# Performance work log

Measured on AMD Instinct MI355X. Metric: run time of the kernel, lower is better.

The kernel has to match this reference:

```python
import jax, jax.numpy as jnp
import numpy as np

EPS = 1e-12  # matches torch F.normalize eps

def _l2_normalize(x):
    n = jnp.linalg.norm(x, axis=-1, keepdims=True)
    return x / jnp.maximum(n, EPS)

def setup_inputs() -> dict:
    key = jax.random.key(0)
    k1, k2, k3 = jax.random.split(key, 3)
    B, D, C = 2048, 1024, 65536
    return {
        "query": jax.random.normal(k1, (B, D), dtype=jnp.float32),
        "memory_keys": jax.random.normal(k2, (C, D), dtype=jnp.float32),
        "memory_values": jax.random.normal(k3, (C, D), dtype=jnp.float32),
        "memory_usage": jnp.zeros((C,), dtype=jnp.float32),
        "k": 8,
    }

def reference(query, memory_keys, memory_values, memory_usage, k):
    # cosine similarity: [B, C]
    qn = _l2_normalize(query)
    mn = _l2_normalize(memory_keys)
    sims = jnp.matmul(qn, mn.T)
    # top-k indices per query: [B, k]
    _, indices = jax.lax.top_k(sims, k)
    # gather retrieved keys/values: [B, k, D]
    retrieved_keys = memory_keys[indices]
    retrieved_values = memory_values[indices]
    # usage scatter-add (+1 per retrieved slot), vectorized form of the loop
    capacity = memory_usage.shape[0]
    counts = jax.ops.segment_sum(
        jnp.ones(indices.size, dtype=memory_usage.dtype),
        indices.reshape(-1),
        num_segments=capacity,
    )
    usage_new = memory_usage + counts
    return retrieved_keys, retrieved_values, usage_new
```

## Files before the change

kernel.cpp:

```cpp
#include <hip/hip_runtime.h>
#include <math.h>

#define BQ 2048
#define DD 1024
#define CC 65536
#define KSEL 8
#define NSTRIPE 32
#define SC (CC / NSTRIPE)
#define GTM 128
#define GTN 128
#define GBK 32
#define NTILES (SC / GTN)
#define LCAND 8
#define TRES 32

typedef unsigned int u32;
typedef unsigned short ushort_t;
typedef __attribute__((ext_vector_type(8))) short bf16x8;
typedef __attribute__((ext_vector_type(4))) float f32x4;


__device__ __forceinline__ ushort_t f2bf(float f) {
    u32 u = __builtin_bit_cast(u32, f);
    return (ushort_t)((u + 0x7FFFu + ((u >> 16) & 1u)) >> 16);
}

__device__ __forceinline__ void gl_lds16(const ushort_t* g, ushort_t* l) {
    __builtin_amdgcn_global_load_lds(
        (const __attribute__((address_space(1))) u32*)g,
        (__attribute__((address_space(3))) u32*)l, 16, 0, 0);
}

__global__ __launch_bounds__(256) void norms_kernel(
    const float* __restrict__ q, const float* __restrict__ keys,
    double* __restrict__ qinv, double* __restrict__ kinv)
{
    const int gtid = blockIdx.x * 256 + threadIdx.x;
    const int wave = gtid >> 6;
    const int lane = threadIdx.x & 63;
    const float4* src;
    double* dst;
    if (wave < CC) {
        src = (const float4*)(keys + (size_t)wave * DD);
        dst = kinv + wave;
    } else {
        const int r = wave - CC;
        if (r >= BQ) return;
        src = (const float4*)(q + (size_t)r * DD);
        dst = qinv + r;
    }
    double s = 0.0;
#pragma unroll
    for (int u = 0; u < 4; ++u) {
        float4 v = src[lane + 64 * u];
        s += (double)v.x * v.x + (double)v.y * v.y +
             (double)v.z * v.z + (double)v.w * v.w;
    }
    for (int off = 32; off > 0; off >>= 1) s += __shfl_down(s, off);
    if (lane == 0) {
        double n = sqrt(s);
        *dst = 1.0 / fmax(n, 1e-12);
    }
}

__global__ __launch_bounds__(256) void convert_kernel(
    const float* __restrict__ q, const float* __restrict__ keys,
    const double* __restrict__ qinv, const double* __restrict__ kinv,
    ushort_t* __restrict__ qn, ushort_t* __restrict__ kn)
{
    const int row = blockIdx.x;
    const int t = threadIdx.x;
    const float4* src;
    ushort_t* dst;
    float inv;
    if (row < CC) {
        src = (const float4*)(keys + (size_t)row * DD);
        dst = kn + (size_t)row * DD;
        inv = (float)kinv[row];
    } else {
        const int r = row - CC;
        src = (const float4*)(q + (size_t)r * DD);
        dst = qn + (size_t)r * DD;
        inv = (float)qinv[r];
    }
    float4 v = src[t];
    ushort4 o;
    o.x = f2bf(v.x * inv); o.y = f2bf(v.y * inv);
    o.z = f2bf(v.z * inv); o.w = f2bf(v.w * inv);
    ((ushort4*)dst)[t] = o;
}

__global__ __launch_bounds__(256, 2) void gemm_topk_kernel(
    const ushort_t* __restrict__ qn, const ushort_t* __restrict__ kn,
    unsigned* __restrict__ cand)
{
    __shared__ ushort_t As[GTM * GBK];
    __shared__ ushort_t Bs[GTN * GBK];
    __shared__ float tilebuf[GTM][65];

    const int tid = threadIdx.x;
    const int wid = tid >> 6;
    const int lane = tid & 63;
    const int wy = wid >> 1, wx = wid & 1;
    const int l15 = lane & 15, quad = lane >> 4;
    const int m0 = blockIdx.x * GTM;
    const int sbase = blockIdx.y * SC;

    const int e0 = tid, e1 = tid + 256;
    const ushort_t* gA0 = qn + (size_t)(m0 + (e0 >> 2)) * DD + (e0 & 3) * 8;
    const ushort_t* gA1 = qn + (size_t)(m0 + (e1 >> 2)) * DD + (e1 & 3) * 8;
    ushort_t* lA0 = As + e0 * 8;
    ushort_t* lA1 = As + e1 * 8;
    ushort_t* lB0 = Bs + e0 * 8;
    ushort_t* lB1 = Bs + e1 * 8;

    float tv[LCAND];
    int ti[LCAND];
#pragma unroll
    for (int l = 0; l < LCAND; ++l) { tv[l] = -3.0e38f; ti[l] = 0; }
    float minv = -3.0e38f;
    int minpos = 0;

    for (int nt = 0; nt < NTILES; ++nt) {
        const int cbase = sbase + nt * GTN;
        const ushort_t* gB0 = kn + (size_t)(cbase + (e0 >> 2)) * DD + (e0 & 3) * 8;
        const ushort_t* gB1 = kn + (size_t)(cbase + (e1 >> 2)) * DD + (e1 & 3) * 8;

        f32x4 acc[4][4];
#pragma unroll
        for (int i = 0; i < 4; ++i)
#pragma unroll
            for (int j = 0; j < 4; ++j) acc[i][j] = (f32x4)0.0f;

        for (int kt = 0; kt < DD / GBK; ++kt) {
            const int k0 = kt * GBK;
            __syncthreads();
            gl_lds16(gA0 + k0, lA0);
            gl_lds16(gA1 + k0, lA1);
            gl_lds16(gB0 + k0, lB0);
            gl_lds16(gB1 + k0, lB1);
            __syncthreads();

            bf16x8 af[4], bfr[4];
#pragma unroll
            for (int ri = 0; ri < 4; ++ri)
                af[ri] = *(const bf16x8*)(As + (wy * 64 + ri * 16 + l15) * GBK + quad * 8);
#pragma unroll
            for (int ci = 0; ci < 4; ++ci)
                bfr[ci] = *(const bf16x8*)(Bs + (wx * 64 + ci * 16 + l15) * GBK + quad * 8);
#pragma unroll
            for (int ri = 0; ri < 4; ++ri)
#pragma unroll
                for (int ci = 0; ci < 4; ++ci)
                    acc[ri][ci] = __builtin_amdgcn_mfma_f32_16x16x32_bf16(
                        af[ri], bfr[ci], acc[ri][ci], 0, 0, 0);
        }

        for (int cc2 = 0; cc2 < 2; ++cc2) {
            __syncthreads();
            if (wx == cc2) {
#pragma unroll
                for (int ri = 0; ri < 4; ++ri)
#pragma unroll
                    for (int ci = 0; ci < 4; ++ci)
#pragma unroll
                        for (int r = 0; r < 4; ++r)
                            tilebuf[wy * 64 + ri * 16 + quad * 4 + r][ci * 16 + l15] =
                                acc[ri][ci][r];
            }
            __syncthreads();
            if (tid < GTM) {
                const int gc0 = cbase + cc2 * 64;
                for (int j = 0; j < 64; ++j) {
                    float v = tilebuf[tid][j];
                    if (v > minv) {
                        tv[minpos] = v; ti[minpos] = gc0 + j;
                        minv = tv[0]; minpos = 0;
#pragma unroll
                        for (int l = 1; l < LCAND; ++l)
                            if (tv[l] < minv) { minv = tv[l]; minpos = l; }
                    }
                }
            }
        }
    }

    if (tid < GTM) {
        unsigned* dst = cand + (size_t)(m0 + tid) * (NSTRIPE * LCAND) + blockIdx.y * LCAND;
#pragma unroll
        for (int l = 0; l < LCAND; ++l)
            dst[l] = ((unsigned)f2bf(tv[l]) << 16) | (unsigned)(ti[l] & 0xFFFF);
    }
}

__global__ __launch_bounds__(256) void merge_kernel(
    const int* __restrict__ cand, int* __restrict__ sel_idx,
    float* __restrict__ counts)
{
    const int gid = blockIdx.x * 256 + threadIdx.x;
    if (gid < CC) counts[gid] = 0.0f;
    const int row = gid >> 6;
    const int lane = threadIdx.x & 63;
    const int* cv = cand + (size_t)row * (NSTRIPE * LCAND);
    int v[4];
#pragma unroll
    for (int u = 0; u < 4; ++u) v[u] = cv[lane + 64 * u];
    for (int r = 0; r < TRES; ++r) {
        int bv = v[0];
#pragma unroll
        for (int u = 1; u < 4; ++u) bv = max(bv, v[u]);
#pragma unroll
        for (int off = 1; off < 64; off <<= 1) bv = max(bv, __shfl_xor(bv, off));
#pragma unroll
        for (int u = 0; u < 4; ++u)
            if (v[u] == bv) v[u] = (int)0x80000000;
        if (lane == 0) sel_idx[row * TRES + r] = bv & 0xFFFF;
    }
}

__global__ __launch_bounds__(256) void rescore_kernel(
    const float* __restrict__ q, const float* __restrict__ keys,
    const double* __restrict__ qinv, const double* __restrict__ kinv,
    const int* __restrict__ sel_idx, double* __restrict__ sel_val)
{
    const int pair = (blockIdx.x * 256 + threadIdx.x) >> 6;
    const int lane = threadIdx.x & 63;
    const int b = pair >> 5;
    const int c = sel_idx[pair];
    const float4* qr = (const float4*)(q + (size_t)b * DD);
    const float4* kr = (const float4*)(keys + (size_t)c * DD);
    double s = 0.0;
#pragma unroll
    for (int u = 0; u < 4; ++u) {
        float4 a = qr[lane + 64 * u];
        float4 k4 = kr[lane + 64 * u];
        s += (double)a.x * k4.x + (double)a.y * k4.y +
             (double)a.z * k4.z + (double)a.w * k4.w;
    }
    for (int off = 32; off > 0; off >>= 1) s += __shfl_down(s, off);
    if (lane == 0) sel_val[pair] = s * qinv[b] * kinv[c];
}

__global__ __launch_bounds__(256) void finalize_kernel(
    const double* __restrict__ sel_val, const int* __restrict__ sel_idx,
    int* __restrict__ topk_idx, float* __restrict__ counts)
{
    const int b = blockIdx.x * 256 + threadIdx.x;
    if (b >= BQ) return;
    double bv[KSEL]; int bi[KSEL];
#pragma unroll
    for (int j = 0; j < KSEL; ++j) { bv[j] = -1.0e300; bi[j] = 0x7fffffff; }
    for (int t = 0; t < TRES; ++t) {
        double v = sel_val[b * TRES + t];
        int idx = sel_idx[b * TRES + t];
        int p = KSEL;
        while (p > 0 && (v > bv[p - 1] || (v == bv[p - 1] && idx < bi[p - 1]))) --p;
        if (p < KSEL) {
            for (int s = KSEL - 1; s > p; --s) { bv[s] = bv[s - 1]; bi[s] = bi[s - 1]; }
            bv[p] = v; bi[p] = idx;
        }
    }
    for (int j = 0; j < KSEL; ++j) {
        topk_idx[b * KSEL + j] = bi[j];
        atomicAdd(&counts[bi[j]], 1.0f);
    }
}

__global__ __launch_bounds__(256) void gather_kernel(
    const float* __restrict__ keys, const float* __restrict__ values,
    const int* __restrict__ topk_idx, float* __restrict__ out_k,
    float* __restrict__ out_v)
{
    const int pair = blockIdx.x;
    const int c = topk_idx[pair];
    const int t = threadIdx.x;
    const float4* ks = (const float4*)(keys + (size_t)c * DD);
    const float4* vs = (const float4*)(values + (size_t)c * DD);
    float4* ok = (float4*)out_k + (size_t)pair * (DD / 4);
    float4* ov = (float4*)out_v + (size_t)pair * (DD / 4);
    ok[t] = ks[t];
    ov[t] = vs[t];
}

__global__ __launch_bounds__(256) void usage_kernel(
    const float* __restrict__ usage_in, const float* __restrict__ counts,
    float* __restrict__ out_u)
{
    const int c = blockIdx.x * 256 + threadIdx.x;
    out_u[c] = usage_in[c] + counts[c];
}

extern "C" void kernel_launch(void* const* d_in, const int* in_sizes, int n_in,
                              void* d_out, int out_size, void* d_ws, size_t ws_size,
                              hipStream_t stream)
{
    const float* q      = (const float*)d_in[0];
    const float* keys   = (const float*)d_in[1];
    const float* values = (const float*)d_in[2];
    const float* usage  = (const float*)d_in[3];

    char* ws = (char*)d_ws;
    double* qinv     = (double*)(ws + 0);
    double* kinv     = (double*)(ws + 16384);
    ushort_t* qn     = (ushort_t*)(ws + 540672);
    float* counts    = (float*)(ws + 540672);
    int* sel_idx     = (int*)(ws + 802816);
    double* sel_val  = (double*)(ws + 1064960);
    int* topk        = (int*)(ws + 1589248);
    unsigned* cand   = (unsigned*)(ws + 4734976);

    float* out_k = (float*)d_out;
    float* out_v = out_k + (size_t)BQ * KSEL * DD;
    float* out_u = out_v + (size_t)BQ * KSEL * DD;
    ushort_t* kn = (ushort_t*)d_out;

    norms_kernel<<<(CC + BQ) / 4, 256, 0, stream>>>(q, keys, qinv, kinv);

    convert_kernel<<<CC + BQ, 256, 0, stream>>>(q, keys, qinv, kinv, qn, kn);

    dim3 g2(BQ / GTM, NSTRIPE);
    gemm_topk_kernel<<<g2, 256, 0, stream>>>(qn, kn, cand);

    merge_kernel<<<BQ / 4, 256, 0, stream>>>((const int*)cand, sel_idx, counts);

    rescore_kernel<<<(BQ * TRES) / 4, 256, 0, stream>>>(q, keys, qinv, kinv,
                                                        sel_idx, sel_val);

    finalize_kernel<<<BQ / 256, 256, 0, stream>>>(sel_val, sel_idx, topk, counts);

    gather_kernel<<<BQ * KSEL, 256, 0, stream>>>(keys, values, topk, out_k, out_v);

    usage_kernel<<<CC / 256, 256, 0, stream>>>(usage, counts, out_u);
}
```

Baseline: 1.268 ms.

## Fuse norm+convert, double-buffer GEMM LDS with swizzle, split top-k scan across threads

Merges the norm and bf16 conversion kernels into one pass so keys and queries are read once. The GEMM now double-buffers its LDS tiles with async global-to-LDS prefetch of the next k-slice and next N-tile, using vmcnt waits and raw barriers. It also XOR-swizzles the LDS layout to cut bank conflicts, remaps blocks for L2 locality, and raises wave priority around the MFMAs. The per-tile top-k scan uses all 256 threads (two halves of 32 columns each) with a final merge, at the cost of more LDS and fragile hand-written synchronisation.

```diff
diff --git a/kernel.cpp b/kernel.cpp
--- a/kernel.cpp
+++ b/kernel.cpp
@@ -20,6 +20,9 @@
 typedef __attribute__((ext_vector_type(4))) float f32x4;
 
 
+#define FENCE() asm volatile("" ::: "memory")
+#define LGKM0() asm volatile("s_waitcnt lgkmcnt(0)" ::: "memory")
+
 __device__ __forceinline__ ushort_t f2bf(float f) {
     u32 u = __builtin_bit_cast(u32, f);
     return (ushort_t)((u + 0x7FFFu + ((u >> 16) & 1u)) >> 16);
@@ -31,62 +34,34 @@
         (__attribute__((address_space(3))) u32*)l, 16, 0, 0);
 }
 
-__global__ __launch_bounds__(256) void norms_kernel(
+__global__ __launch_bounds__(256) void normconv_kernel(
     const float* __restrict__ q, const float* __restrict__ keys,
-    double* __restrict__ qinv, double* __restrict__ kinv)
-{
-    const int gtid = blockIdx.x * 256 + threadIdx.x;
-    const int wave = gtid >> 6;
-    const int lane = threadIdx.x & 63;
-    const float4* src;
-    double* dst;
-    if (wave < CC) {
-        src = (const float4*)(keys + (size_t)wave * DD);
-        dst = kinv + wave;
-    } else {
-        const int r = wave - CC;
-        if (r >= BQ) return;
-        src = (const float4*)(q + (size_t)r * DD);
-        dst = qinv + r;
-    }
-    double s = 0.0;
-#pragma unroll
-    for (int u = 0; u < 4; ++u) {
-        float4 v = src[lane + 64 * u];
-        s += (double)v.x * v.x + (double)v.y * v.y +
-             (double)v.z * v.z + (double)v.w * v.w;
-    }
-    for (int off = 32; off > 0; off >>= 1) s += __shfl_down(s, off);
-    if (lane == 0) {
-        double n = sqrt(s);
-        *dst = 1.0 / fmax(n, 1e-12);
-    }
-}
-
-__global__ __launch_bounds__(256) void convert_kernel(
-    const float* __restrict__ q, const float* __restrict__ keys,
-    const double* __restrict__ qinv, const double* __restrict__ kinv,
+    double* __restrict__ qinv, double* __restrict__ kinv,
     ushort_t* __restrict__ qn, ushort_t* __restrict__ kn)
 {
+    __shared__ double red[4];
     const int row = blockIdx.x;
     const int t = threadIdx.x;
-    const float4* src;
-    ushort_t* dst;
-    float inv;
-    if (row < CC) {
-        src = (const float4*)(keys + (size_t)row * DD);
-        dst = kn + (size_t)row * DD;
-        inv = (float)kinv[row];
-    } else {
-        const int r = row - CC;
-        src = (const float4*)(q + (size_t)r * DD);
-        dst = qn + (size_t)r * DD;
-        inv = (float)qinv[r];
-    }
-    float4 v = src[t];
+    const bool iskey = row < CC;
+    const float* src = iskey ? keys + (size_t)row * DD
+                             : q + (size_t)(row - CC) * DD;
+    float4 v = ((const float4*)src)[t];
+    double s = (double)v.x * v.x + (double)v.y * v.y +
+               (double)v.z * v.z + (double)v.w * v.w;
+    for (int off = 32; off > 0; off >>= 1) s += __shfl_down(s, off);
+    if ((t & 63) == 0) red[t >> 6] = s;
+    __syncthreads();
+    const double tot = red[0] + red[1] + red[2] + red[3];
+    const double inv = 1.0 / fmax(sqrt(tot), 1e-12);
+    if (t == 0) {
+        if (iskey) kinv[row] = inv; else qinv[row - CC] = inv;
+    }
+    const float invf = (float)inv;
     ushort4 o;
-    o.x = f2bf(v.x * inv); o.y = f2bf(v.y * inv);
-    o.z = f2bf(v.z * inv); o.w = f2bf(v.w * inv);
+    o.x = f2bf(v.x * invf); o.y = f2bf(v.y * invf);
+    o.z = f2bf(v.z * invf); o.w = f2bf(v.w * invf);
+    ushort_t* dst = iskey ? kn + (size_t)row * DD
+                          : qn + (size_t)(row - CC) * DD;
     ((ushort4*)dst)[t] = o;
 }
 
@@ -94,8 +69,8 @@
     const ushort_t* __restrict__ qn, const ushort_t* __restrict__ kn,
     unsigned* __restrict__ cand)
 {
-    __shared__ ushort_t As[GTM * GBK];
-    __shared__ ushort_t Bs[GTN * GBK];
+    __shared__ ushort_t As[2][GTM * GBK];
+    __shared__ ushort_t Bs[2][GTN * GBK];
     __shared__ float tilebuf[GTM][65];
 
     const int tid = threadIdx.x;
@@ -103,16 +78,27 @@
     const int lane = tid & 63;
     const int wy = wid >> 1, wx = wid & 1;
     const int l15 = lane & 15, quad = lane >> 4;
-    const int m0 = blockIdx.x * GTM;
-    const int sbase = blockIdx.y * SC;
+
+    const int flat = blockIdx.y * 16 + blockIdx.x;
+    const int swz  = (flat & 7) * 64 + (flat >> 3);
+    const int bx = swz & 15, by = swz >> 4;
+    const int m0 = bx * GTM;
+    const int sbase = by * SC;
 
     const int e0 = tid, e1 = tid + 256;
-    const ushort_t* gA0 = qn + (size_t)(m0 + (e0 >> 2)) * DD + (e0 & 3) * 8;
-    const ushort_t* gA1 = qn + (size_t)(m0 + (e1 >> 2)) * DD + (e1 & 3) * 8;
-    ushort_t* lA0 = As + e0 * 8;
-    ushort_t* lA1 = As + e1 * 8;
-    ushort_t* lB0 = Bs + e0 * 8;
-    ushort_t* lB1 = Bs + e1 * 8;
+    const int ks0 = (((e0 & 3) ^ ((e0 >> 3) & 3)) * 8);
+    const int ks1 = (((e1 & 3) ^ ((e1 >> 3) & 3)) * 8);
+    const ushort_t* gA0 = qn + (size_t)(m0 + (e0 >> 2)) * DD + ks0;
+    const ushort_t* gA1 = qn + (size_t)(m0 + (e1 >> 2)) * DD + ks1;
+    const ushort_t* gB0 = kn + (size_t)(sbase + (e0 >> 2)) * DD + ks0;
+    const ushort_t* gB1 = kn + (size_t)(sbase + (e1 >> 2)) * DD + ks1;
+
+#define STAGE(buf, k0_) do {                         \
+        gl_lds16(gA0 + (k0_), As[buf] + e0 * 8);     \
+        gl_lds16(gA1 + (k0_), As[buf] + e1 * 8);     \
+        gl_lds16(gB0 + (k0_), Bs[buf] + e0 * 8);     \
+        gl_lds16(gB1 + (k0_), Bs[buf] + e1 * 8);     \
+    } while (0)
 
     float tv[LCAND];
     int ti[LCAND];
@@ -121,10 +107,12 @@
     float minv = -3.0e38f;
     int minpos = 0;
 
+    const int swz15 = (l15 >> 1) & 3;
+
+    STAGE(0, 0);
+
     for (int nt = 0; nt < NTILES; ++nt) {
         const int cbase = sbase + nt * GTN;
-        const ushort_t* gB0 = kn + (size_t)(cbase + (e0 >> 2)) * DD + (e0 & 3) * 8;
-        const ushort_t* gB1 = kn + (size_t)(cbase + (e1 >> 2)) * DD + (e1 & 3) * 8;
 
         f32x4 acc[4][4];
 #pragma unroll
@@ -132,32 +120,50 @@
 #pragma unroll
             for (int j = 0; j < 4; ++j) acc[i][j] = (f32x4)0.0f;
 
+#pragma unroll 2
         for (int kt = 0; kt < DD / GBK; ++kt) {
-            const int k0 = kt * GBK;
-            __syncthreads();
-            gl_lds16(gA0 + k0, lA0);
-            gl_lds16(gA1 + k0, lA1);
-            gl_lds16(gB0 + k0, lB0);
-            gl_lds16(gB1 + k0, lB1);
-            __syncthreads();
+            const int cur = kt & 1;
+            if (kt < DD / GBK - 1) {
+                STAGE(cur ^ 1, (kt + 1) * GBK);
+                asm volatile("s_waitcnt vmcnt(4)" ::: "memory");
+            } else if (nt < NTILES - 1) {
+                gB0 += (size_t)GTN * DD;
+                gB1 += (size_t)GTN * DD;
+                STAGE(cur ^ 1, 0);
+                asm volatile("s_waitcnt vmcnt(4)" ::: "memory");
+            } else {
+                asm volatile("s_waitcnt vmcnt(0)" ::: "memory");
+            }
+            __builtin_amdgcn_s_barrier();
+            FENCE();
+            __builtin_amdgcn_s_setprio(1);
 
             bf16x8 af[4], bfr[4];
 #pragma unroll
             for (int ri = 0; ri < 4; ++ri)
-                af[ri] = *(const bf16x8*)(As + (wy * 64 + ri * 16 + l15) * GBK + quad * 8);
+                af[ri] = *(const bf16x8*)(As[cur] +
+                    (wy * 64 + ri * 16 + l15) * GBK + ((quad ^ swz15) * 8));
 #pragma unroll
             for (int ci = 0; ci < 4; ++ci)
-                bfr[ci] = *(const bf16x8*)(Bs + (wx * 64 + ci * 16 + l15) * GBK + quad * 8);
+                bfr[ci] = *(const bf16x8*)(Bs[cur] +
+                    (wx * 64 + ci * 16 + l15) * GBK + ((quad ^ swz15) * 8));
 #pragma unroll
             for (int ri = 0; ri < 4; ++ri)
 #pragma unroll
                 for (int ci = 0; ci < 4; ++ci)
                     acc[ri][ci] = __builtin_amdgcn_mfma_f32_16x16x32_bf16(
                         af[ri], bfr[ci], acc[ri][ci], 0, 0, 0);
+
+            __builtin_amdgcn_s_setprio(0);
+            FENCE();
+            __builtin_amdgcn_s_barrier();
+            FENCE();
         }
 
         for (int cc2 = 0; cc2 < 2; ++cc2) {
-            __syncthreads();
+            LGKM0();
+            __builtin_amdgcn_s_barrier();
+            FENCE();
             if (wx == cc2) {
 #pragma unroll
                 for (int ri = 0; ri < 4; ++ri)
@@ -168,11 +174,15 @@
                             tilebuf[wy * 64 + ri * 16 + quad * 4 + r][ci * 16 + l15] =
                                 acc[ri][ci][r];
             }
-            __syncthreads();
-            if (tid < GTM) {
-                const int gc0 = cbase + cc2 * 64;
-                for (int j = 0; j < 64; ++j) {
-                    float v = tilebuf[tid][j];
+            LGKM0();
+            __builtin_amdgcn_s_barrier();
+            FENCE();
+            {
+                const int rr = tid & 127;
+                const int jb = (tid >> 7) << 5;
+                const int gc0 = cbase + cc2 * 64 + jb;
+                for (int j = 0; j < 32; ++j) {
+                    float v = tilebuf[rr][jb + j];
                     if (v > minv) {
                         tv[minpos] = v; ti[minpos] = gc0 + j;
                         minv = tv[0]; minpos = 0;
@@ -185,12 +195,39 @@
         }
     }
 
+    LGKM0();
+    __builtin_amdgcn_s_barrier();
+    FENCE();
+    if (tid >= 128) {
+        const int r2 = tid - 128;
+#pragma unroll
+        for (int l = 0; l < LCAND; ++l) {
+            tilebuf[r2][l] = tv[l];
+            tilebuf[r2][16 + l] = __int_as_float(ti[l]);
+        }
+    }
+    LGKM0();
+    __builtin_amdgcn_s_barrier();
+    FENCE();
     if (tid < GTM) {
-        unsigned* dst = cand + (size_t)(m0 + tid) * (NSTRIPE * LCAND) + blockIdx.y * LCAND;
+#pragma unroll
+        for (int c = 0; c < LCAND; ++c) {
+            float v = tilebuf[tid][c];
+            int idx = __float_as_int(tilebuf[tid][16 + c]);
+            if (v > minv) {
+                tv[minpos] = v; ti[minpos] = idx;
+                minv = tv[0]; minpos = 0;
+#pragma unroll
+                for (int l = 1; l < LCAND; ++l)
+                    if (tv[l] < minv) { minv = tv[l]; minpos = l; }
+            }
+        }
+        unsigned* dst = cand + (size_t)(m0 + tid) * (NSTRIPE * LCAND) + by * LCAND;
 #pragma unroll
         for (int l = 0; l < LCAND; ++l)
             dst[l] = ((unsigned)f2bf(tv[l]) << 16) | (unsigned)(ti[l] & 0xFFFF);
     }
+#undef STAGE
 }
 
 __global__ __launch_bounds__(256) void merge_kernel(
@@ -314,9 +351,7 @@
     float* out_u = out_v + (size_t)BQ * KSEL * DD;
     ushort_t* kn = (ushort_t*)d_out;
 
-    norms_kernel<<<(CC + BQ) / 4, 256, 0, stream>>>(q, keys, qinv, kinv);
-
-    convert_kernel<<<CC + BQ, 256, 0, stream>>>(q, keys, qinv, kinv, qn, kn);
+    normconv_kernel<<<CC + BQ, 256, 0, stream>>>(q, keys, qinv, kinv, qn, kn);
 
     dim3 g2(BQ / GTM, NSTRIPE);
     gemm_topk_kernel<<<g2, 256, 0, stream>>>(qn, kn, cand);
```

Result: faster. 1.129 ms (-11.0%).
